# Optimization experiments

Measured on AMD Instinct MI355X. Metric: run time of the kernel, lower is better.

Reference implementation:

```python
import jax, jax.numpy as jnp
import numpy as np

N = 50000
E = 800000
IN_C = 128
HID = 128
OUT_C = 2


def _linear_params(key, fan_in, fan_out):
    k1, k2 = jax.random.split(key)
    bound = 1.0 / np.sqrt(fan_in)
    W = jax.random.uniform(k1, (fan_in, fan_out), jnp.float32, -bound, bound)
    b = jax.random.uniform(k2, (fan_out,), jnp.float32, -bound, bound)
    return W, b


def setup_inputs() -> dict:
    key = jax.random.key(0)
    ks = jax.random.split(key, 9)
    x = jax.random.normal(ks[0], (N, IN_C), jnp.float32)
    edge_index = jax.random.randint(ks[1], (2, E), 0, N, jnp.int64)
    W1a, b1a = _linear_params(ks[2], IN_C, HID)
    W1b, b1b = _linear_params(ks[3], HID, HID)
    W2a, b2a = _linear_params(ks[4], HID, HID)
    W2b, b2b = _linear_params(ks[5], HID, HID)
    Wfc, bfc = _linear_params(ks[6], HID, OUT_C)
    return {
        "x": x, "edge_index": edge_index,
        "W1a": W1a, "b1a": b1a, "W1b": W1b, "b1b": b1b,
        "W2a": W2a, "b2a": b2a, "W2b": W2b, "b2b": b2b,
        "Wfc": Wfc, "bfc": bfc,
    }


def _gin_conv(x, src, dst, Wa, ba, Wb, bb):
    # GINConv with eps=0: h = MLP(x + sum_{j in N(i)} x_j)
    agg = jax.ops.segment_sum(x[src], dst, num_segments=N)  # [N, d]
    h = x + agg
    h = jax.nn.relu(h @ Wa + ba)
    return h @ Wb + bb


def reference(x, edge_index, W1a, b1a, W1b, b1b, W2a, b2a, W2b, b2b, Wfc, bfc):
    src, dst = edge_index[0], edge_index[1]  # messages flow src -> dst
    h = _gin_conv(x, src, dst, W1a, b1a, W1b, b1b)
    h = jax.nn.relu(h)
    # dropout is identity in eval mode
    h = _gin_conv(h, src, dst, W2a, b2a, W2b, b2b)
    return h @ Wfc + bfc  # [N, 2]
```

## Files before the change

kernel.cpp:

```cpp
#include <hip/hip_runtime.h>

#define N_NODES 50000
#define N_EDGES 800000
#define NBUK    392
#define B_A     1024
#define EPB     782
#define CAPB    2560

typedef unsigned short u16;
typedef unsigned int   u32;
typedef __bf16 bf16x8 __attribute__((ext_vector_type(8)));
typedef float  f32x4  __attribute__((ext_vector_type(4)));

__device__ __forceinline__ float bf_lo(u32 v){ return __uint_as_float(v << 16); }
__device__ __forceinline__ float bf_hi(u32 v){ return __uint_as_float(v & 0xffff0000u); }
__device__ __forceinline__ u32 bf_pack(float a, float b){
    u32 ua = __float_as_uint(a), ub = __float_as_uint(b);
    ua += 0x7fffu + ((ua >> 16) & 1u);
    ub += 0x7fffu + ((ub >> 16) & 1u);
    return (ua >> 16) | (ub & 0xffff0000u);
}
__device__ __forceinline__ u16 f2bf(float a){
    u32 ua = __float_as_uint(a);
    ua += 0x7fffu + ((ua >> 16) & 1u);
    return (u16)(ua >> 16);
}
__device__ __forceinline__ void addu4(uint4 v, float* a){
    a[0] += bf_lo(v.x); a[1] += bf_hi(v.x);
    a[2] += bf_lo(v.y); a[3] += bf_hi(v.y);
    a[4] += bf_lo(v.z); a[5] += bf_hi(v.z);
    a[6] += bf_lo(v.w); a[7] += bf_hi(v.w);
}

__device__ __forceinline__ int blockScan256(int v, int* ws, int t) {
    int lane = t & 63, w = t >> 6;
    #pragma unroll
    for (int off = 1; off < 64; off <<= 1) {
        int u = __shfl_up(v, off);
        if (lane >= off) v += u;
    }
    if (lane == 63) ws[w] = v;
    __syncthreads();
    int add = 0;
    for (int k = 0; k < w; k++) add += ws[k];
    return v + add;
}

__device__ __forceinline__ int blockScan512(int v, int* ws, int t) {
    int lane = t & 63, w = t >> 6;
    #pragma unroll
    for (int off = 1; off < 64; off <<= 1) {
        int u = __shfl_up(v, off);
        if (lane >= off) v += u;
    }
    if (lane == 63) ws[w] = v;
    __syncthreads();
    int add = 0;
    for (int k = 0; k < w; k++) add += ws[k];
    return v + add;
}

__launch_bounds__(256)
__global__ void binA_kernel(const int* __restrict__ esrc, const int* __restrict__ edst,
                            u32* __restrict__ binned, int* __restrict__ startTab,
                            int* __restrict__ cntTab,
                            const float* __restrict__ xsrc, u32* __restrict__ xb,
                            const float* __restrict__ W1a, const float* __restrict__ W1b,
                            const float* __restrict__ W2a, const float* __restrict__ W2b,
                            const float* __restrict__ Wfc, const float* __restrict__ b2b,
                            const float* __restrict__ bfc,
                            u16* __restrict__ wt1a, u16* __restrict__ wt1b,
                            u16* __restrict__ wt2a,
                            float* __restrict__ Wc, float* __restrict__ bc) {
    int t = threadIdx.x, blk = blockIdx.x;
    if (blk >= B_A) {
        int b = blk - B_A;
        if (b < 192) {
            int g  = b * 256 + t;
            int mi = g >> 14;
            int p  = g & 16383;
            int k  = p >> 7, m = p & 127;
            const float* src = (mi == 0) ? W1a : (mi == 1) ? W1b : W2a;
            u16* dst         = (mi == 0) ? wt1a : (mi == 1) ? wt1b : wt2a;
            dst[m * 128 + k] = f2bf(src[k * 128 + m]);
        } else {
            int j = t >> 1, o = t & 1;
            float s = 0.f;
            for (int k = 0; k < 128; k++)
                s += W2b[j * 128 + k] * Wfc[k * 2 + o];
            Wc[j * 2 + o] = s;
            if (t < 2) {
                float s2 = 0.f;
                for (int k = 0; k < 128; k++)
                    s2 += b2b[k] * Wfc[k * 2 + t];
                bc[t] = s2 + bfc[t];
            }
        }
        return;
    }
    __shared__ int hist[NBUK];
    __shared__ int cur[NBUK];
    __shared__ u32 ebuf[EPB];
    __shared__ int ws[4];
    int base = blk * EPB;
    for (int i = t; i < NBUK; i += 256) hist[i] = 0;
    __syncthreads();
    for (int i = t; i < EPB; i += 256) {
        int gi = base + i;
        if (gi < N_EDGES) atomicAdd(&hist[edst[gi] >> 7], 1);
    }
    __syncthreads();
    int c0 = 0, c1 = 0;
    if (t < 196) { c0 = hist[2 * t]; c1 = hist[2 * t + 1]; }
    int s2 = c0 + c1;
    int incl = blockScan256(s2, ws, t);
    int excl = incl - s2;
    if (t < 196) {
        startTab[(2 * t) * B_A + blk]     = excl;
        cntTab[(2 * t) * B_A + blk]       = c0;
        cur[2 * t] = excl;
        startTab[(2 * t + 1) * B_A + blk] = excl + c0;
        cntTab[(2 * t + 1) * B_A + blk]   = c1;
        cur[2 * t + 1] = excl + c0;
    }
    __syncthreads();
    for (int i = t; i < EPB; i += 256) {
        int gi = base + i;
        if (gi < N_EDGES) {
            int d = edst[gi], s = esrc[gi];
            int p = atomicAdd(&cur[d >> 7], 1);
            ebuf[p] = (u32)s | ((u32)(d & 127) << 16);
        }
    }
    __syncthreads();
    for (int i = t; i < EPB; i += 256)
        binned[base + i] = ebuf[i];
    const int total = N_NODES * 64;
    for (int i = blk * 256 + t; i < total; i += B_A * 256) {
        float2 f = ((const float2*)xsrc)[i];
        xb[i] = bf_pack(f.x, f.y);
    }
}

__launch_bounds__(512, 4)
__global__ void bconv1_kernel(const u32* __restrict__ binned,
                              const int* __restrict__ startTab, const int* __restrict__ cntTab,
                              const u32* __restrict__ xb,
                              const u16* __restrict__ WA, const float* __restrict__ bA,
                              const u16* __restrict__ WB, const float* __restrict__ bB,
                              int2* __restrict__ span, int* __restrict__ csr,
                              u16* __restrict__ h1, int n) {
    __shared__ __align__(16) char shbuf[34816 + 10240 + 512 + 512 + 32 + 16];
    u16 (*As)[136] = (u16(*)[136])shbuf;
    u32* ebuf      = (u32*)shbuf;
    int* cbuf      = (int*)(shbuf + 34816);
    int* hist      = (int*)(shbuf + 34816 + 10240);
    int* cursor    = (int*)(shbuf + 34816 + 10240 + 512);
    int* ws        = (int*)(shbuf + 34816 + 10240 + 1024);
    int* totsh     = ws + 8;
    int b = blockIdx.x, t = threadIdx.x;

    int c2[2], rs2[2], s = 0;
    #pragma unroll
    for (int q = 0; q < 2; q++) {
        int run = t * 2 + q;
        c2[q]  = cntTab[b * B_A + run];
        rs2[q] = run * EPB + startTab[b * B_A + run];
        s += c2[q];
    }
    int incl = blockScan512(s, ws, t);
    int rb = incl - s;
    if (t == 511) *totsh = incl;
    if (t < 128) hist[t] = 0;
    __syncthreads();
    #pragma unroll
    for (int q = 0; q < 2; q++) {
        int c = c2[q], rs = rs2[q];
        for (int k = 0; k < c; k++) {
            int p = rb + k;
            if (p < CAPB) ebuf[p] = binned[rs + k];
        }
        rb += c;
    }
    __syncthreads();
    int tot = *totsh;
    if (tot > CAPB) tot = CAPB;
    for (int i = t; i < tot; i += 512)
        atomicAdd(&hist[ebuf[i] >> 16], 1);
    __syncthreads();
    int hv = (t < 128) ? hist[t] : 0;
    int hincl = blockScan512(hv, ws, t);
    int hexcl = hincl - hv;
    int gb = b * CAPB;
    if (t < 128) {
        hist[t]   = hexcl;
        cursor[t] = hexcl;
        int node = (b << 7) + t;
        if (node < n) span[node] = make_int2(gb + hexcl, gb + hexcl + hv);
    }
    __syncthreads();
    for (int i = t; i < tot; i += 512) {
        u32 e = ebuf[i];
        int p = atomicAdd(&cursor[e >> 16], 1);
        cbuf[p] = (int)(e & 0xFFFFu);
    }
    __syncthreads();
    for (int i = t; i < tot; i += 512)
        csr[gb + i] = cbuf[i];
    __syncthreads();

    int row0 = b * 128;
    int w = t >> 6, lane = t & 63;
    int g4 = lane >> 4, l16 = lane & 15;
    const uint4* xp = (const uint4*)xb;
    #pragma unroll
    for (int p = 0; p < 4; p++) {
        int rl = w * 16 + p * 4 + g4;
        int node = row0 + rl;
        float a[8] = {0.f,0.f,0.f,0.f,0.f,0.f,0.f,0.f};
        if (node < n) {
            addu4(xp[(size_t)node * 16 + l16], a);
            int j = hist[rl], jend = cursor[rl];
            for (; j + 4 <= jend; j += 4) {
                int s0 = cbuf[j], s1 = cbuf[j + 1], s2b = cbuf[j + 2], s3 = cbuf[j + 3];
                uint4 v0 = xp[(size_t)s0 * 16 + l16], v1 = xp[(size_t)s1 * 16 + l16];
                uint4 v2 = xp[(size_t)s2b * 16 + l16], v3 = xp[(size_t)s3 * 16 + l16];
                addu4(v0, a); addu4(v1, a); addu4(v2, a); addu4(v3, a);
            }
            for (; j < jend; j++)
                addu4(xp[(size_t)cbuf[j] * 16 + l16], a);
        }
        uint4 pk = make_uint4(bf_pack(a[0], a[1]), bf_pack(a[2], a[3]),
                              bf_pack(a[4], a[5]), bf_pack(a[6], a[7]));
        *(uint4*)&As[rl][l16 * 8] = pk;
    }
    int lm = l16, lq = g4;
    f32x4 acc[8];
    #pragma unroll
    for (int c = 0; c < 8; c++) acc[c] = (f32x4){0.f, 0.f, 0.f, 0.f};
    #pragma unroll
    for (int kk = 0; kk < 4; kk++) {
        bf16x8 af = *(const bf16x8*)&As[w * 16 + lm][kk * 32 + lq * 8];
        #pragma unroll
        for (int c = 0; c < 8; c++) {
            bf16x8 bf = *(const bf16x8*)(WA + (size_t)(c * 16 + lm) * 128 + kk * 32 + lq * 8);
            acc[c] = __builtin_amdgcn_mfma_f32_16x16x32_bf16(af, bf, acc[c], 0, 0, 0);
        }
    }
    #pragma unroll
    for (int c = 0; c < 8; c++) {
        int col = c * 16 + lm;
        float bcol = bA[col];
        #pragma unroll
        for (int r = 0; r < 4; r++) {
            float v = acc[c][r] + bcol;
            v = v > 0.f ? v : 0.f;
            As[w * 16 + lq * 4 + r][col] = f2bf(v);
        }
    }
    f32x4 acc2[8];
    #pragma unroll
    for (int c = 0; c < 8; c++) acc2[c] = (f32x4){0.f, 0.f, 0.f, 0.f};
    #pragma unroll
    for (int kk = 0; kk < 4; kk++) {
        bf16x8 af = *(const bf16x8*)&As[w * 16 + lm][kk * 32 + lq * 8];
        #pragma unroll
        for (int c = 0; c < 8; c++) {
            bf16x8 bf = *(const bf16x8*)(WB + (size_t)(c * 16 + lm) * 128 + kk * 32 + lq * 8);
            acc2[c] = __builtin_amdgcn_mfma_f32_16x16x32_bf16(af, bf, acc2[c], 0, 0, 0);
        }
    }
    #pragma unroll
    for (int c = 0; c < 8; c++) {
        int col = c * 16 + lm;
        float bcol = bB[col];
        #pragma unroll
        for (int r = 0; r < 4; r++) {
            int row = row0 + w * 16 + lq * 4 + r;
            if (row < n) {
                float v = acc2[c][r] + bcol;
                v = v > 0.f ? v : 0.f;
                h1[(size_t)row * 128 + col] = f2bf(v);
            }
        }
    }
}

__launch_bounds__(256, 4)
__global__ void fconv2_kernel(const u32* __restrict__ xb,
                              const u16* __restrict__ WA, const float* __restrict__ bA,
                              const float* __restrict__ Wc, const float* __restrict__ bc,
                              const int2* __restrict__ span, const int* __restrict__ csr,
                              float2* __restrict__ out, int n) {
    __shared__ u16 As[64][136];
    int t = threadIdx.x;
    int row0 = blockIdx.x * 64;
    int w = t >> 6, lane = t & 63;
    int g4 = lane >> 4, l16 = lane & 15;
    const uint4* xp = (const uint4*)xb;
    #pragma unroll
    for (int p = 0; p < 4; p++) {
        int rl = w * 16 + p * 4 + g4;
        int node = row0 + rl;
        float a[8] = {0.f,0.f,0.f,0.f,0.f,0.f,0.f,0.f};
        if (node < n) {
            addu4(xp[(size_t)node * 16 + l16], a);
            int2 sp = span[node];
            int j = sp.x, jend = sp.y;
            for (; j + 4 <= jend; j += 4) {
                int s0 = csr[j], s1 = csr[j + 1], s2 = csr[j + 2], s3 = csr[j + 3];
                uint4 v0 = xp[(size_t)s0 * 16 + l16], v1 = xp[(size_t)s1 * 16 + l16];
                uint4 v2 = xp[(size_t)s2 * 16 + l16], v3 = xp[(size_t)s3 * 16 + l16];
                addu4(v0, a); addu4(v1, a); addu4(v2, a); addu4(v3, a);
            }
            for (; j < jend; j++)
                addu4(xp[(size_t)csr[j] * 16 + l16], a);
        }
        uint4 pk = make_uint4(bf_pack(a[0], a[1]), bf_pack(a[2], a[3]),
                              bf_pack(a[4], a[5]), bf_pack(a[6], a[7]));
        *(uint4*)&As[rl][l16 * 8] = pk;
    }
    int lm = l16, lq = g4;
    f32x4 acc[8];
    #pragma unroll
    for (int c = 0; c < 8; c++) acc[c] = (f32x4){0.f, 0.f, 0.f, 0.f};
    #pragma unroll
    for (int kk = 0; kk < 4; kk++) {
        bf16x8 af = *(const bf16x8*)&As[w * 16 + lm][kk * 32 + lq * 8];
        #pragma unroll
        for (int c = 0; c < 8; c++) {
            bf16x8 bf = *(const bf16x8*)(WA + (size_t)(c * 16 + lm) * 128 + kk * 32 + lq * 8);
            acc[c] = __builtin_amdgcn_mfma_f32_16x16x32_bf16(af, bf, acc[c], 0, 0, 0);
        }
    }
    float p0[4] = {0,0,0,0}, p1[4] = {0,0,0,0};
    #pragma unroll
    for (int c = 0; c < 8; c++) {
        int col = c * 16 + lm;
        float bcol = bA[col];
        float2 wc = ((const float2*)Wc)[col];
        #pragma unroll
        for (int r = 0; r < 4; r++) {
            float v = acc[c][r] + bcol;
            v = v > 0.f ? v : 0.f;
            p0[r] += v * wc.x;
            p1[r] += v * wc.y;
        }
    }
    #pragma unroll
    for (int off = 1; off < 16; off <<= 1) {
        #pragma unroll
        for (int r = 0; r < 4; r++) {
            p0[r] += __shfl_xor(p0[r], off);
            p1[r] += __shfl_xor(p1[r], off);
        }
    }
    if (lm == 0) {
        float b0 = bc[0], b1 = bc[1];
        #pragma unroll
        for (int r = 0; r < 4; r++) {
            int row = row0 + w * 16 + lq * 4 + r;
            if (row < n) out[row] = make_float2(p0[r] + b0, p1[r] + b1);
        }
    }
}

extern "C" void kernel_launch(void* const* d_in, const int* in_sizes, int n_in,
                              void* d_out, int out_size, void* d_ws, size_t ws_size,
                              hipStream_t stream) {
    const float* x   = (const float*)d_in[0];
    const int*   ei  = (const int*)d_in[1];
    const float* W1a = (const float*)d_in[2];
    const float* b1a = (const float*)d_in[3];
    const float* W1b = (const float*)d_in[4];
    const float* b1b = (const float*)d_in[5];
    const float* W2a = (const float*)d_in[6];
    const float* b2a = (const float*)d_in[7];
    const float* W2b = (const float*)d_in[8];
    const float* b2b = (const float*)d_in[9];
    const float* Wfc = (const float*)d_in[10];
    const float* bfc = (const float*)d_in[11];

    const int* esrc = ei;
    const int* edst = ei + N_EDGES;

    char* w = (char*)d_ws;
    size_t off = 0;
    auto alloc = [&](size_t bytes) -> char* {
        char* p = w + off;
        off = (off + bytes + 255) & ~(size_t)255;
        return p;
    };
    int2*  span       = (int2*)alloc((size_t)N_NODES * 8);
    int*   startTab   = (int*)alloc((size_t)NBUK * B_A * 4);
    int*   cntTab     = (int*)alloc((size_t)NBUK * B_A * 4);
    int*   csr        = (int*)alloc((size_t)NBUK * CAPB * 4);
    u32*   binned     = (u32*)alloc((size_t)B_A * EPB * 4);
    u16*   wt1a       = (u16*)alloc(128 * 128 * 2);
    u16*   wt1b       = (u16*)alloc(128 * 128 * 2);
    u16*   wt2a       = (u16*)alloc(128 * 128 * 2);
    float* Wc         = (float*)alloc(256 * 4);
    float* bc         = (float*)alloc(2 * 4);
    u16*   bufA       = (u16*)alloc((size_t)N_NODES * 128 * 2);
    u16*   bufB       = (u16*)alloc((size_t)N_NODES * 128 * 2);

    binA_kernel<<<B_A + 193, 256, 0, stream>>>(esrc, edst, binned, startTab, cntTab,
                                               x, (u32*)bufB,
                                               W1a, W1b, W2a, W2b, Wfc, b2b, bfc,
                                               wt1a, wt1b, wt2a, Wc, bc);
    bconv1_kernel<<<NBUK, 512, 0, stream>>>(binned, startTab, cntTab,
                                            (const u32*)bufB, wt1a, b1a, wt1b, b1b,
                                            span, csr, bufA, N_NODES);
    fconv2_kernel<<<(N_NODES + 63) / 64, 256, 0, stream>>>((const u32*)bufA, wt2a, b2a,
                                                           Wc, bc, span, csr,
                                                           (float2*)d_out, N_NODES);
}
```

Before: 214.0 us.

## Split node features into 32-column slabs for cache-friendlier gather passes

Stores the bf16 node features and the layer-1 output as four column slabs of 32 channels each, instead of interleaved 128-channel rows. Both aggregation kernels now gather one slab at a time in four passes, with 4 lanes per node and 16 nodes per wave. Each pass touches a smaller working set (about 3.2 MB per slab), so gathered rows are more likely to stay in L2. The cost is re-reading the CSR indices four times, a block-wide barrier after every pass, and 64-byte rather than 256-byte contiguous reads per neighbor.

Result: slower. 226.4 us (+5.8%).

```diff
diff --git a/kernel.cpp b/kernel.cpp
--- a/kernel.cpp
+++ b/kernel.cpp
@@ -6,6 +6,8 @@
 #define B_A     1024
 #define EPB     782
 #define CAPB    2560
+#define SLAB32  (N_NODES * 16)
+#define SLAB16  (N_NODES * 32)
 
 typedef unsigned short u16;
 typedef unsigned int   u32;
@@ -138,7 +140,8 @@
     const int total = N_NODES * 64;
     for (int i = blk * 256 + t; i < total; i += B_A * 256) {
         float2 f = ((const float2*)xsrc)[i];
-        xb[i] = bf_pack(f.x, f.y);
+        int node = i >> 6, c2 = i & 63;
+        xb[(c2 >> 4) * SLAB32 + node * 16 + (c2 & 15)] = bf_pack(f.x, f.y);
     }
 }
 
@@ -211,30 +214,33 @@
 
     int row0 = b * 128;
     int w = t >> 6, lane = t & 63;
-    int g4 = lane >> 4, l16 = lane & 15;
-    const uint4* xp = (const uint4*)xb;
-    #pragma unroll
-    for (int p = 0; p < 4; p++) {
-        int rl = w * 16 + p * 4 + g4;
-        int node = row0 + rl;
+    int sub = lane >> 2, ch = lane & 3;
+    int rl = w * 16 + sub;
+    int node = row0 + rl;
+    int jb = hist[rl], je = cursor[rl];
+    #pragma unroll
+    for (int pass = 0; pass < 4; pass++) {
+        const uint4* sp = (const uint4*)(xb + pass * SLAB32);
         float a[8] = {0.f,0.f,0.f,0.f,0.f,0.f,0.f,0.f};
         if (node < n) {
-            addu4(xp[(size_t)node * 16 + l16], a);
-            int j = hist[rl], jend = cursor[rl];
-            for (; j + 4 <= jend; j += 4) {
+            addu4(sp[node * 4 + ch], a);
+            int j = jb;
+            for (; j + 4 <= je; j += 4) {
                 int s0 = cbuf[j], s1 = cbuf[j + 1], s2b = cbuf[j + 2], s3 = cbuf[j + 3];
-                uint4 v0 = xp[(size_t)s0 * 16 + l16], v1 = xp[(size_t)s1 * 16 + l16];
-                uint4 v2 = xp[(size_t)s2b * 16 + l16], v3 = xp[(size_t)s3 * 16 + l16];
+                uint4 v0 = sp[s0 * 4 + ch], v1 = sp[s1 * 4 + ch];
+                uint4 v2 = sp[s2b * 4 + ch], v3 = sp[s3 * 4 + ch];
                 addu4(v0, a); addu4(v1, a); addu4(v2, a); addu4(v3, a);
             }
-            for (; j < jend; j++)
-                addu4(xp[(size_t)cbuf[j] * 16 + l16], a);
+            for (; j < je; j++)
+                addu4(sp[cbuf[j] * 4 + ch], a);
         }
         uint4 pk = make_uint4(bf_pack(a[0], a[1]), bf_pack(a[2], a[3]),
                               bf_pack(a[4], a[5]), bf_pack(a[6], a[7]));
-        *(uint4*)&As[rl][l16 * 8] = pk;
-    }
-    int lm = l16, lq = g4;
+        *(uint4*)&As[rl][pass * 32 + ch * 8] = pk;
+        __syncthreads();
+    }
+
+    int lm = lane & 15, lq = lane >> 4;
     f32x4 acc[8];
     #pragma unroll
     for (int c = 0; c < 8; c++) acc[c] = (f32x4){0.f, 0.f, 0.f, 0.f};
@@ -274,20 +280,21 @@
     for (int c = 0; c < 8; c++) {
         int col = c * 16 + lm;
         float bcol = bB[col];
+        int slab = col >> 5, cw = col & 31;
         #pragma unroll
         for (int r = 0; r < 4; r++) {
             int row = row0 + w * 16 + lq * 4 + r;
             if (row < n) {
                 float v = acc2[c][r] + bcol;
                 v = v > 0.f ? v : 0.f;
-                h1[(size_t)row * 128 + col] = f2bf(v);
+                h1[slab * SLAB16 + row * 32 + cw] = f2bf(v);
             }
         }
     }
 }
 
 __launch_bounds__(256, 4)
-__global__ void fconv2_kernel(const u32* __restrict__ xb,
+__global__ void fconv2_kernel(const u32* __restrict__ h1,
                               const u16* __restrict__ WA, const float* __restrict__ bA,
                               const float* __restrict__ Wc, const float* __restrict__ bc,
                               const int2* __restrict__ span, const int* __restrict__ csr,
@@ -296,31 +303,33 @@
     int t = threadIdx.x;
     int row0 = blockIdx.x * 64;
     int w = t >> 6, lane = t & 63;
-    int g4 = lane >> 4, l16 = lane & 15;
-    const uint4* xp = (const uint4*)xb;
-    #pragma unroll
-    for (int p = 0; p < 4; p++) {
-        int rl = w * 16 + p * 4 + g4;
-        int node = row0 + rl;
+    int sub = lane >> 2, ch = lane & 3;
+    int rl = w * 16 + sub;
+    int node = row0 + rl;
+    int jb = 0, je = 0;
+    if (node < n) { int2 sp0 = span[node]; jb = sp0.x; je = sp0.y; }
+    #pragma unroll
+    for (int pass = 0; pass < 4; pass++) {
+        const uint4* sp = (const uint4*)(h1 + pass * SLAB32);
         float a[8] = {0.f,0.f,0.f,0.f,0.f,0.f,0.f,0.f};
         if (node < n) {
-            addu4(xp[(size_t)node * 16 + l16], a);
-            int2 sp = span[node];
-            int j = sp.x, jend = sp.y;
-            for (; j + 4 <= jend; j += 4) {
+            addu4(sp[node * 4 + ch], a);
+            int j = jb;
+            for (; j + 4 <= je; j += 4) {
                 int s0 = csr[j], s1 = csr[j + 1], s2 = csr[j + 2], s3 = csr[j + 3];
-                uint4 v0 = xp[(size_t)s0 * 16 + l16], v1 = xp[(size_t)s1 * 16 + l16];
-                uint4 v2 = xp[(size_t)s2 * 16 + l16], v3 = xp[(size_t)s3 * 16 + l16];
+                uint4 v0 = sp[s0 * 4 + ch], v1 = sp[s1 * 4 + ch];
+                uint4 v2 = sp[s2 * 4 + ch], v3 = sp[s3 * 4 + ch];
                 addu4(v0, a); addu4(v1, a); addu4(v2, a); addu4(v3, a);
             }
-            for (; j < jend; j++)
-                addu4(xp[(size_t)csr[j] * 16 + l16], a);
+            for (; j < je; j++)
+                addu4(sp[csr[j] * 4 + ch], a);
         }
         uint4 pk = make_uint4(bf_pack(a[0], a[1]), bf_pack(a[2], a[3]),
                               bf_pack(a[4], a[5]), bf_pack(a[6], a[7]));
-        *(uint4*)&As[rl][l16 * 8] = pk;
-    }
-    int lm = l16, lq = g4;
+        *(uint4*)&As[rl][pass * 32 + ch * 8] = pk;
+        __syncthreads();
+    }
+    int lm = lane & 15, lq = lane >> 4;
     f32x4 acc[8];
     #pragma unroll
     for (int c = 0; c < 8; c++) acc[c] = (f32x4){0.f, 0.f, 0.f, 0.f};
```
